# Kernel optimization log

Measured on AMD Instinct MI355X. Metric: run time of the kernel, lower is better.

The kernel has to match this reference:

```python
import jax, jax.numpy as jnp
import numpy as np

B, S, E, H, P = 8, 1024, 768, 12, 64
MASKED = True

def setup_inputs() -> dict:
    key = jax.random.key(0)
    k1, k2, k3, k4, k5 = jax.random.split(key, 5)
    scale = 0.02  # keep softmax logits in a sane range
    return {
        "x": jax.random.normal(k1, (B, 1, S, E), dtype=jnp.float32),
        "key_proj": jax.random.normal(k2, (H, E, P), dtype=jnp.float32) * scale,
        "value_proj": jax.random.normal(k3, (H, E, P), dtype=jnp.float32) * scale,
        "q_heads": jax.random.normal(k4, (H, S, S), dtype=jnp.float32) * scale,
        "lifting": jax.random.normal(k5, (1, H * P, E), dtype=jnp.float32) * scale,
    }

def reference(x, key_proj, value_proj, q_heads, lifting):
    # x: (B,1,S,E); key/value_proj: (H,E,P) -> broadcast matmul gives (B,H,S,P)
    k = jnp.matmul(x, key_proj)            # (B,H,S,P)
    v = jnp.matmul(x, value_proj)          # (B,H,S,P)
    # scores = (q_heads @ v) @ k^T, then transpose last two dims and scale
    qv = jnp.matmul(q_heads, v)            # (B,H,S,P)
    a_ts = jnp.matmul(qv, jnp.swapaxes(k, -2, -1))  # (B,H,S,S)
    a_ts = jnp.swapaxes(a_ts, -2, -1) / np.float32(np.sqrt(E))
    a_t = jax.nn.softmax(a_ts, axis=-1)
    if MASKED:
        a_t = jnp.tril(a_t)                 # causal lower-triangular mask
        a_t = a_t / jnp.sum(a_t, axis=-1, keepdims=True)  # renormalize rows
    attn = jnp.matmul(a_t, v)               # (B,H,S,P)
    attn = jnp.swapaxes(attn, 1, 2).reshape(B, S, H * P)  # (B,S,H*P)
    return jnp.matmul(attn, lifting)         # (B,S,E) via (1,H*P,E) broadcast
```

## Files before the change

kernel.cpp:

```cpp
#include <hip/hip_runtime.h>
#include <hip/hip_bf16.h>
#include <math.h>

#define B_ 8
#define S_ 1024
#define E_ 768
#define H_ 12
#define P_ 64

typedef __attribute__((ext_vector_type(8))) short bf16x8;
typedef __attribute__((ext_vector_type(4))) float f32x4;

__device__ __forceinline__ short f2bf(float f) {
    union { float f; unsigned u; } v; v.f = f;
    unsigned r = v.u + 0x7FFFu + ((v.u >> 16) & 1u);
    return (short)(r >> 16);
}

__device__ __forceinline__ short f2bf_hw(float f) {
    union { __hip_bfloat16 h; short s; } cv;
    cv.h = __float2bfloat16(f);
    return cv.s;
}

__device__ __forceinline__ void conv_T_body(
    const float* __restrict__ src0, short* __restrict__ dst0, int R, int C,
    int bx, int by, int bz, short (*T)[72])
{
    const int t = threadIdx.x;
    const int r0 = bx * 64, c0 = by * 64;
    const size_t bo = (size_t)bz * R * C;
    const float* src = src0 + bo;
    short* dst = dst0 + bo;
#pragma unroll
    for (int i = 0; i < 4; ++i) {
        int id = i * 256 + t;
        int r = id >> 4, c4 = id & 15;
        float4 f = *(const float4*)(src + (size_t)(r0 + r) * C + c0 + c4 * 4);
        T[c4 * 4 + 0][r] = f2bf(f.x);
        T[c4 * 4 + 1][r] = f2bf(f.y);
        T[c4 * 4 + 2][r] = f2bf(f.z);
        T[c4 * 4 + 3][r] = f2bf(f.w);
    }
    __syncthreads();
#pragma unroll
    for (int i = 0; i < 2; ++i) {
        int id = i * 256 + t;
        int cc = id >> 3, r8 = id & 7;
        *(uint4*)(dst + (size_t)(c0 + cc) * R + r0 + r8 * 8) = *(const uint4*)&T[cc][r8 * 8];
    }
}

__global__ __launch_bounds__(256) void conv_fused(
    const float* __restrict__ x, const float* __restrict__ qh,
    const float* __restrict__ kproj, const float* __restrict__ vproj,
    const float* __restrict__ lifting,
    short* __restrict__ xb, short* __restrict__ qhb,
    short* __restrict__ kTw, short* __restrict__ vTw, short* __restrict__ liftT)
{
    __shared__ short T[64][72];
    const int bid = (int)blockIdx.x;
    if (bid < 18432) {
        const float4* src; ushort4* dst; int idx;
        if (bid < 6144) { src = (const float4*)x;  dst = (ushort4*)xb;  idx = bid * 256 + threadIdx.x; }
        else            { src = (const float4*)qh; dst = (ushort4*)qhb; idx = (bid - 6144) * 256 + threadIdx.x; }
        float4 f = src[idx];
        ushort4 u;
        u.x = (unsigned short)f2bf(f.x);
        u.y = (unsigned short)f2bf(f.y);
        u.z = (unsigned short)f2bf(f.z);
        u.w = (unsigned short)f2bf(f.w);
        dst[idx] = u;
    } else if (bid < 18576) {
        int r = bid - 18432;
        conv_T_body(kproj, kTw, E_, P_, r % 12, 0, r / 12, T);
    } else if (bid < 18720) {
        int r = bid - 18576;
        conv_T_body(vproj, vTw, E_, P_, r % 12, 0, r / 12, T);
    } else {
        int r = bid - 18720;
        conv_T_body(lifting, liftT, E_, E_, r % 12, r / 12, 0, T);
    }
}

__device__ __forceinline__ void mfma_gemm_128x128(
    const short* __restrict__ A, int lda,
    const short* __restrict__ B0, const short* __restrict__ B1, int ldb, int K,
    short (*As)[72], short (*Bs)[72], f32x4 (&acc)[2][4])
{
    const int tid = threadIdx.x;
    const int w = tid >> 6, lane = tid & 63, quad = lane >> 4, ln = lane & 15;
    const int wm = w & 3, wn = w >> 2;

    const int r = tid >> 3, c8 = (tid & 7) * 8;
    const short* sA0 = A  + (size_t)r * lda + c8;
    const short* sA1 = A  + (size_t)(r + 64) * lda + c8;
    const short* sB0 = B0 + (size_t)r * ldb + c8;
    const short* sB1 = B1 + (size_t)r * ldb + c8;
    short* dA0 = &As[r][c8];
    short* dA1 = &As[r + 64][c8];
    short* dB0 = &Bs[r][c8];
    short* dB1 = &Bs[r + 64][c8];

    uint4 a0p = *(const uint4*)sA0;
    uint4 a1p = *(const uint4*)sA1;
    uint4 b0p = *(const uint4*)sB0;
    uint4 b1p = *(const uint4*)sB1;

    for (int k0 = 0; k0 < K; k0 += 64) {
        __syncthreads();
        *(uint4*)dA0 = a0p;
        *(uint4*)dA1 = a1p;
        *(uint4*)dB0 = b0p;
        *(uint4*)dB1 = b1p;
        if (k0 + 64 < K) {
            a0p = *(const uint4*)(sA0 + k0 + 64);
            a1p = *(const uint4*)(sA1 + k0 + 64);
            b0p = *(const uint4*)(sB0 + k0 + 64);
            b1p = *(const uint4*)(sB1 + k0 + 64);
        }
        __syncthreads();
#pragma unroll
        for (int kc = 0; kc < 2; ++kc) {
            bf16x8 a0 = *(const bf16x8*)&As[wm * 32 + ln][kc * 32 + quad * 8];
            bf16x8 a1 = *(const bf16x8*)&As[wm * 32 + 16 + ln][kc * 32 + quad * 8];
#pragma unroll
            for (int ni = 0; ni < 4; ++ni) {
                bf16x8 b = *(const bf16x8*)&Bs[wn * 64 + ni * 16 + ln][kc * 32 + quad * 8];
                acc[0][ni] = __builtin_amdgcn_mfma_f32_16x16x32_bf16(a0, b, acc[0][ni], 0, 0, 0);
                acc[1][ni] = __builtin_amdgcn_mfma_f32_16x16x32_bf16(a1, b, acc[1][ni], 0, 0, 0);
            }
        }
    }
}

__global__ __launch_bounds__(512, 2) void proj_kv_mfma(
    const short* __restrict__ xb,
    const short* __restrict__ kTw,
    const short* __restrict__ vTw,
    short* __restrict__ kb,
    short* __restrict__ vTb)
{
    __shared__ short As[128][72];
    __shared__ short Bs[128][72];
    const int tid = threadIdx.x;
    const int w = tid >> 6, lane = tid & 63, quad = lane >> 4, ln = lane & 15;
    const int wm = w & 3, wn = w >> 2;

    const int lid = (int)blockIdx.x;
    const int xcd = lid & 7, s = lid >> 3;
    const int mloc = s & 7, h = s >> 3;
    const int m0 = (xcd * 8 + mloc) * 128;

    f32x4 acc[2][4] = {};
    mfma_gemm_128x128(xb + (size_t)m0 * E_, E_,
                      kTw + (size_t)h * P_ * E_, vTw + (size_t)h * P_ * E_, E_, E_,
                      As, Bs, acc);

    const int b = m0 >> 10;
    const int sbase = (m0 & 1023) + wm * 32;
    if (wn == 0) {
        short* outp = kb + ((size_t)(b * H_ + h)) * S_ * P_;
#pragma unroll
        for (int mi = 0; mi < 2; ++mi)
#pragma unroll
            for (int ni = 0; ni < 4; ++ni)
#pragma unroll
                for (int r = 0; r < 4; ++r) {
                    int ss = sbase + mi * 16 + quad * 4 + r;
                    outp[(size_t)ss * P_ + ni * 16 + ln] = f2bf(acc[mi][ni][r]);
                }
    } else {
        short* outp = vTb + ((size_t)(b * H_ + h)) * P_ * S_;
#pragma unroll
        for (int mi = 0; mi < 2; ++mi)
#pragma unroll
            for (int ni = 0; ni < 4; ++ni) {
                int p = ni * 16 + ln;
                int ss = sbase + mi * 16 + quad * 4;
                ushort4 u;
                u.x = (unsigned short)f2bf(acc[mi][ni][0]);
                u.y = (unsigned short)f2bf(acc[mi][ni][1]);
                u.z = (unsigned short)f2bf(acc[mi][ni][2]);
                u.w = (unsigned short)f2bf(acc[mi][ni][3]);
                *(ushort4*)(outp + (size_t)p * S_ + ss) = u;
            }
    }
}

__global__ __launch_bounds__(512, 2) void qv_mfma(
    const short* __restrict__ qhb,
    const short* __restrict__ vTb,
    short* __restrict__ qvb)
{
    __shared__ short As[128][72];
    __shared__ short Bs[128][72];
    const int tid = threadIdx.x;
    const int w = tid >> 6, lane = tid & 63, quad = lane >> 4, ln = lane & 15;
    const int wm = w & 3, wn = w >> 2;

    const int lid = (int)blockIdx.x;
    const int xcd = lid & 7, s = lid >> 3;
    const int virt = xcd * 48 + s;
    const int h = virt >> 5;
    const int rem = virt & 31;
    const int mt = rem >> 2, bp = rem & 3;
    const int m0 = mt * 128;

    const short* Bv0 = vTb + (size_t)((bp * 2 + 0) * H_ + h) * P_ * S_;
    const short* Bv1 = vTb + (size_t)((bp * 2 + 1) * H_ + h) * P_ * S_;

    f32x4 acc[2][4] = {};
    mfma_gemm_128x128(qhb + (size_t)h * S_ * S_ + (size_t)m0 * S_, S_,
                      Bv0, Bv1, S_, S_, As, Bs, acc);

    const int b = bp * 2 + wn;
    short* outp = qvb + (size_t)(b * H_ + h) * S_ * P_;
#pragma unroll
    for (int mi = 0; mi < 2; ++mi)
#pragma unroll
        for (int ni = 0; ni < 4; ++ni)
#pragma unroll
            for (int r = 0; r < 4; ++r) {
                int ss = m0 + wm * 32 + mi * 16 + quad * 4 + r;
                outp[(size_t)ss * P_ + ni * 16 + ln] = f2bf(acc[mi][ni][r]);
            }
}

__global__ __launch_bounds__(512, 4) void flash_mfma(
    const short* __restrict__ kb,
    const short* __restrict__ qvb,
    const short* __restrict__ vTb,
    short* __restrict__ attn2)
{
    __shared__ short Ks[64][72];
    __shared__ short Vts[64][72];
    __shared__ short Ps[8][16][72];

    const int tid = threadIdx.x;
    const int w = tid >> 6, lane = tid & 63, quad = lane >> 4, ln = lane & 15;
    const int wq = w & 3;
    const int wsel = w >> 2;

    const int lid = (int)blockIdx.x;
    const int xcd = lid & 7, sl = lid >> 3;
    const int bh  = xcd * 12 + (sl >> 3);
    const int pair = sl & 7;
    const int qhi = 15 - pair;
    const int qb  = wsel ? pair : qhi;
    const int b = bh / H_, h = bh % H_;

    const short* Q  = kb  + (size_t)bh * S_ * P_ + ((size_t)qb * 64 + wq * 16) * P_;
    const short* K  = qvb + (size_t)bh * S_ * P_;
    const short* Vt = vTb + (size_t)bh * P_ * S_;

    bf16x8 qf[2];
    qf[0] = *(const bf16x8*)(Q + (size_t)ln * P_ + quad * 8);
    qf[1] = *(const bf16x8*)(Q + (size_t)ln * P_ + 32 + quad * 8);

    const int krow = tid >> 3, kc8 = (tid & 7) * 8;
    const short* Kst = K + (size_t)krow * P_ + kc8;
    const short* Vst = Vt + (size_t)krow * S_ + kc8;
    uint4 rK = *(const uint4*)Kst;
    uint4 rV = *(const uint4*)Vst;

    f32x4 o[4] = {};
    float l[4] = {};
    short (*Pw)[72] = Ps[w];
    const float c2 = 0.03608439182435161f * 1.4426950408889634f;
    const int rowbase = wq * 16;

    for (int jt = 0; jt <= qhi; ++jt) {
        __syncthreads();
        *(uint4*)&Ks[krow][kc8] = rK;
        *(uint4*)&Vts[krow][kc8] = rV;
        if (jt < qhi) {
            rK = *(const uint4*)(Kst + (size_t)(jt + 1) * 64 * P_);
            rV = *(const uint4*)(Vst + (jt + 1) * 64);
        }
        __syncthreads();

        if (jt <= qb) {
            const bool diag = (jt == qb);
            f32x4 s[4] = {};
#pragma unroll
            for (int kc = 0; kc < 2; ++kc)
#pragma unroll
                for (int ni = 0; ni < 4; ++ni) {
                    bf16x8 kf = *(const bf16x8*)&Ks[ni * 16 + ln][kc * 32 + quad * 8];
                    s[ni] = __builtin_amdgcn_mfma_f32_16x16x32_bf16(qf[kc], kf, s[ni], 0, 0, 0);
                }

#pragma unroll
            for (int r = 0; r < 4; ++r) {
                const int row = quad * 4 + r;
                float p[4];
#pragma unroll
                for (int ni = 0; ni < 4; ++ni) {
                    float v = __builtin_amdgcn_exp2f(c2 * s[ni][r]);
                    if (diag && (ni * 16 + ln) > (rowbase + row)) v = 0.f;
                    p[ni] = v;
                    l[r] += v;
                }
#pragma unroll
                for (int ni = 0; ni < 4; ++ni)
                    Pw[row][ni * 16 + ln] = f2bf_hw(p[ni]);
            }

#pragma unroll
            for (int kc = 0; kc < 2; ++kc) {
                bf16x8 pa = *(const bf16x8*)&Pw[ln][kc * 32 + quad * 8];
#pragma unroll
                for (int ni = 0; ni < 4; ++ni) {
                    bf16x8 vb = *(const bf16x8*)&Vts[ni * 16 + ln][kc * 32 + quad * 8];
                    o[ni] = __builtin_amdgcn_mfma_f32_16x16x32_bf16(pa, vb, o[ni], 0, 0, 0);
                }
            }
        }
    }

#pragma unroll
    for (int r = 0; r < 4; ++r) {
        float lv = l[r];
#pragma unroll
        for (int off = 1; off < 16; off <<= 1)
            lv += __shfl_xor(lv, off, 16);
        float inv = 1.0f / lv;
        int gi = qb * 64 + rowbase + quad * 4 + r;
#pragma unroll
        for (int ni = 0; ni < 4; ++ni)
            attn2[((size_t)b * S_ + gi) * (H_ * P_) + h * P_ + ni * 16 + ln] =
                f2bf(o[ni][r] * inv);
    }
}

__global__ __launch_bounds__(512, 2) void lift_mfma(
    const short* __restrict__ attn2,
    const short* __restrict__ liftT,
    float* __restrict__ outp)
{
    __shared__ short As[128][72];
    __shared__ short Bs[128][72];
    const int tid = threadIdx.x;
    const int w = tid >> 6, lane = tid & 63, quad = lane >> 4, ln = lane & 15;
    const int wm = w & 3, wn = w >> 2;

    const int lid = (int)blockIdx.x;
    const int xcd = lid & 7, s = lid >> 3;
    const int mloc = s & 7, np = s >> 3;
    const int m0 = (xcd * 8 + mloc) * 128;
    const int n0 = np * 128;

    f32x4 acc[2][4] = {};
    mfma_gemm_128x128(attn2 + (size_t)m0 * E_, E_,
                      liftT + (size_t)n0 * E_, liftT + (size_t)(n0 + 64) * E_, E_, E_,
                      As, Bs, acc);

#pragma unroll
    for (int mi = 0; mi < 2; ++mi)
#pragma unroll
        for (int ni = 0; ni < 4; ++ni)
#pragma unroll
            for (int r = 0; r < 4; ++r) {
                int m = m0 + wm * 32 + mi * 16 + quad * 4 + r;
                outp[(size_t)m * E_ + n0 + wn * 64 + ni * 16 + ln] = acc[mi][ni][r];
            }
}

extern "C" void kernel_launch(void* const* d_in, const int* in_sizes, int n_in,
                              void* d_out, int out_size, void* d_ws, size_t ws_size,
                              hipStream_t stream) {
    (void)in_sizes; (void)n_in; (void)out_size; (void)ws_size;
    const float* x       = (const float*)d_in[0];
    const float* kproj   = (const float*)d_in[1];
    const float* vproj   = (const float*)d_in[2];
    const float* qheads  = (const float*)d_in[3];
    const float* lifting = (const float*)d_in[4];
    float* out = (float*)d_out;

    short* ws = (short*)d_ws;
    const size_t N_X   = (size_t)B_ * S_ * E_;
    const size_t N_QH  = (size_t)H_ * S_ * S_;
    const size_t N_W   = (size_t)H_ * P_ * E_;
    const size_t N_L   = (size_t)E_ * E_;
    const size_t N_KV  = (size_t)B_ * H_ * S_ * P_;

    short* xb    = ws;                 ws += N_X;
    short* qhb   = ws;                 ws += N_QH;
    short* kTw   = ws;                 ws += N_W;
    short* vTw   = ws;                 ws += N_W;
    short* liftT = ws;                 ws += N_L;
    short* kb    = ws;                 ws += N_KV;
    short* vTb   = ws;                 ws += N_KV;
    short* qvb   = ws;                 ws += N_KV;
    short* attn2 = ws;                 ws += N_KV;

    conv_fused<<<dim3(18864), 256, 0, stream>>>(x, qheads, kproj, vproj, lifting,
                                                xb, qhb, kTw, vTw, liftT);
    proj_kv_mfma<<<dim3(768), 512, 0, stream>>>(xb, kTw, vTw, kb, vTb);
    qv_mfma<<<dim3(384), 512, 0, stream>>>(qhb, vTb, qvb);
    flash_mfma<<<dim3(768), 512, 0, stream>>>(kb, qvb, vTb, attn2);
    lift_mfma<<<dim3(384), 512, 0, stream>>>(attn2, liftT, out);
}
```

Measured before the change: 219.8 us.

## Rebalance flash kernel: split long query block's tail across both wave groups

Before, each block paired a short query tile (pair) with a long one (qhi), and the short tile's four waves sat idle once their causal range ended. Now both wave groups share the first phase. Once the short tile finishes, its waves write it out and switch to the long tile, with each group computing half of the key columns per KV tile. The two halves' partial O and l are then reduced through shared memory. This adds an extra barrier per tile in the second phase plus a final LDS reduction, and lowers launch bounds occupancy from 4 to 2.

```diff
diff --git a/kernel.cpp b/kernel.cpp
--- a/kernel.cpp
+++ b/kernel.cpp
@@ -227,7 +227,7 @@
             }
 }
 
-__global__ __launch_bounds__(512, 4) void flash_mfma(
+__global__ __launch_bounds__(512, 2) void flash_mfma(
     const short* __restrict__ kb,
     const short* __restrict__ qvb,
     const short* __restrict__ vTb,
@@ -235,7 +235,10 @@
 {
     __shared__ short Ks[64][72];
     __shared__ short Vts[64][72];
-    __shared__ short Ps[8][16][72];
+    __shared__ union PU {
+        short ps[8][16][72];
+        struct { float ored[4][16][68]; float lred[4][16][17]; } red;
+    } pu;
 
     const int tid = threadIdx.x;
     const int w = tid >> 6, lane = tid & 63, quad = lane >> 4, ln = lane & 15;
@@ -247,13 +250,14 @@
     const int bh  = xcd * 12 + (sl >> 3);
     const int pair = sl & 7;
     const int qhi = 15 - pair;
-    const int qb  = wsel ? pair : qhi;
     const int b = bh / H_, h = bh % H_;
 
-    const short* Q  = kb  + (size_t)bh * S_ * P_ + ((size_t)qb * 64 + wq * 16) * P_;
+    const short* Qbase = kb + (size_t)bh * S_ * P_;
     const short* K  = qvb + (size_t)bh * S_ * P_;
     const short* Vt = vTb + (size_t)bh * P_ * S_;
 
+    const int qb0 = wsel ? pair : qhi;
+    const short* Q = Qbase + ((size_t)qb0 * 64 + wq * 16) * P_;
     bf16x8 qf[2];
     qf[0] = *(const bf16x8*)(Q + (size_t)ln * P_ + quad * 8);
     qf[1] = *(const bf16x8*)(Q + (size_t)ln * P_ + 32 + quad * 8);
@@ -266,11 +270,78 @@
 
     f32x4 o[4] = {};
     float l[4] = {};
-    short (*Pw)[72] = Ps[w];
+    short (*Pw)[72] = pu.ps[w];
     const float c2 = 0.03608439182435161f * 1.4426950408889634f;
     const int rowbase = wq * 16;
 
-    for (int jt = 0; jt <= qhi; ++jt) {
+    for (int jt = 0; jt <= pair; ++jt) {
+        __syncthreads();
+        *(uint4*)&Ks[krow][kc8] = rK;
+        *(uint4*)&Vts[krow][kc8] = rV;
+        rK = *(const uint4*)(Kst + (size_t)(jt + 1) * 64 * P_);
+        rV = *(const uint4*)(Vst + (jt + 1) * 64);
+        __syncthreads();
+
+        const bool diag = (wsel == 1) && (jt == pair);
+        f32x4 s[4] = {};
+#pragma unroll
+        for (int kc = 0; kc < 2; ++kc)
+#pragma unroll
+            for (int ni = 0; ni < 4; ++ni) {
+                bf16x8 kf = *(const bf16x8*)&Ks[ni * 16 + ln][kc * 32 + quad * 8];
+                s[ni] = __builtin_amdgcn_mfma_f32_16x16x32_bf16(qf[kc], kf, s[ni], 0, 0, 0);
+            }
+#pragma unroll
+        for (int r = 0; r < 4; ++r) {
+            const int row = quad * 4 + r;
+            float p[4];
+#pragma unroll
+            for (int ni = 0; ni < 4; ++ni) {
+                float v = __builtin_amdgcn_exp2f(c2 * s[ni][r]);
+                if (diag && (ni * 16 + ln) > (rowbase + row)) v = 0.f;
+                p[ni] = v;
+                l[r] += v;
+            }
+#pragma unroll
+            for (int ni = 0; ni < 4; ++ni)
+                Pw[row][ni * 16 + ln] = f2bf_hw(p[ni]);
+        }
+#pragma unroll
+        for (int kc = 0; kc < 2; ++kc) {
+            bf16x8 pa = *(const bf16x8*)&Pw[ln][kc * 32 + quad * 8];
+#pragma unroll
+            for (int ni = 0; ni < 4; ++ni) {
+                bf16x8 vb = *(const bf16x8*)&Vts[ni * 16 + ln][kc * 32 + quad * 8];
+                o[ni] = __builtin_amdgcn_mfma_f32_16x16x32_bf16(pa, vb, o[ni], 0, 0, 0);
+            }
+        }
+    }
+
+    if (wsel == 1) {
+#pragma unroll
+        for (int r = 0; r < 4; ++r) {
+            float lv = l[r];
+#pragma unroll
+            for (int off = 1; off < 16; off <<= 1)
+                lv += __shfl_xor(lv, off, 16);
+            float inv = 1.0f / lv;
+            int gi = pair * 64 + rowbase + quad * 4 + r;
+#pragma unroll
+            for (int ni = 0; ni < 4; ++ni)
+                attn2[((size_t)b * S_ + gi) * (H_ * P_) + h * P_ + ni * 16 + ln] =
+                    f2bf(o[ni][r] * inv);
+        }
+#pragma unroll
+        for (int ni = 0; ni < 4; ++ni) o[ni] = (f32x4){0.f, 0.f, 0.f, 0.f};
+#pragma unroll
+        for (int r = 0; r < 4; ++r) l[r] = 0.f;
+        const short* Qh = Qbase + ((size_t)qhi * 64 + wq * 16) * P_;
+        qf[0] = *(const bf16x8*)(Qh + (size_t)ln * P_ + quad * 8);
+        qf[1] = *(const bf16x8*)(Qh + (size_t)ln * P_ + 32 + quad * 8);
+    }
+
+    short (*Pq)[72] = pu.ps[wq];
+    for (int jt = pair + 1; jt <= qhi; ++jt) {
         __syncthreads();
         *(uint4*)&Ks[krow][kc8] = rK;
         *(uint4*)&Vts[krow][kc8] = rV;
@@ -280,57 +351,75 @@
         }
         __syncthreads();
 
-        if (jt <= qb) {
-            const bool diag = (jt == qb);
-            f32x4 s[4] = {};
-#pragma unroll
-            for (int kc = 0; kc < 2; ++kc)
-#pragma unroll
-                for (int ni = 0; ni < 4; ++ni) {
-                    bf16x8 kf = *(const bf16x8*)&Ks[ni * 16 + ln][kc * 32 + quad * 8];
-                    s[ni] = __builtin_amdgcn_mfma_f32_16x16x32_bf16(qf[kc], kf, s[ni], 0, 0, 0);
-                }
-
-#pragma unroll
-            for (int r = 0; r < 4; ++r) {
-                const int row = quad * 4 + r;
-                float p[4];
-#pragma unroll
-                for (int ni = 0; ni < 4; ++ni) {
-                    float v = __builtin_amdgcn_exp2f(c2 * s[ni][r]);
-                    if (diag && (ni * 16 + ln) > (rowbase + row)) v = 0.f;
-                    p[ni] = v;
-                    l[r] += v;
-                }
-#pragma unroll
-                for (int ni = 0; ni < 4; ++ni)
-                    Pw[row][ni * 16 + ln] = f2bf_hw(p[ni]);
-            }
-
-#pragma unroll
-            for (int kc = 0; kc < 2; ++kc) {
-                bf16x8 pa = *(const bf16x8*)&Pw[ln][kc * 32 + quad * 8];
-#pragma unroll
-                for (int ni = 0; ni < 4; ++ni) {
-                    bf16x8 vb = *(const bf16x8*)&Vts[ni * 16 + ln][kc * 32 + quad * 8];
-                    o[ni] = __builtin_amdgcn_mfma_f32_16x16x32_bf16(pa, vb, o[ni], 0, 0, 0);
-                }
-            }
-        }
-    }
-
-#pragma unroll
-    for (int r = 0; r < 4; ++r) {
-        float lv = l[r];
-#pragma unroll
-        for (int off = 1; off < 16; off <<= 1)
-            lv += __shfl_xor(lv, off, 16);
-        float inv = 1.0f / lv;
-        int gi = qb * 64 + rowbase + quad * 4 + r;
-#pragma unroll
-        for (int ni = 0; ni < 4; ++ni)
-            attn2[((size_t)b * S_ + gi) * (H_ * P_) + h * P_ + ni * 16 + ln] =
-                f2bf(o[ni][r] * inv);
+        const bool diag = (jt == qhi);
+        f32x4 s2[2] = {};
+#pragma unroll
+        for (int kc = 0; kc < 2; ++kc)
+#pragma unroll
+            for (int nii = 0; nii < 2; ++nii) {
+                const int ni = wsel * 2 + nii;
+                bf16x8 kf = *(const bf16x8*)&Ks[ni * 16 + ln][kc * 32 + quad * 8];
+                s2[nii] = __builtin_amdgcn_mfma_f32_16x16x32_bf16(qf[kc], kf, s2[nii], 0, 0, 0);
+            }
+#pragma unroll
+        for (int r = 0; r < 4; ++r) {
+            const int row = quad * 4 + r;
+            float p[2];
+#pragma unroll
+            for (int nii = 0; nii < 2; ++nii) {
+                const int col = (wsel * 2 + nii) * 16 + ln;
+                float v = __builtin_amdgcn_exp2f(c2 * s2[nii][r]);
+                if (diag && col > (rowbase + row)) v = 0.f;
+                p[nii] = v;
+                l[r] += v;
+            }
+#pragma unroll
+            for (int nii = 0; nii < 2; ++nii)
+                Pq[row][(wsel * 2 + nii) * 16 + ln] = f2bf_hw(p[nii]);
+        }
+        __syncthreads();
+        {
+            bf16x8 pa = *(const bf16x8*)&Pq[ln][wsel * 32 + quad * 8];
+#pragma unroll
+            for (int ni = 0; ni < 4; ++ni) {
+                bf16x8 vb = *(const bf16x8*)&Vts[ni * 16 + ln][wsel * 32 + quad * 8];
+                o[ni] = __builtin_amdgcn_mfma_f32_16x16x32_bf16(pa, vb, o[ni], 0, 0, 0);
+            }
+        }
+    }
+
+    __syncthreads();
+    if (wsel == 1) {
+#pragma unroll
+        for (int r = 0; r < 4; ++r) {
+            pu.red.lred[wq][quad * 4 + r][ln] = l[r];
+#pragma unroll
+            for (int ni = 0; ni < 4; ++ni)
+                pu.red.ored[wq][quad * 4 + r][ni * 16 + ln] = o[ni][r];
+        }
+    }
+    __syncthreads();
+    if (wsel == 0) {
+#pragma unroll
+        for (int r = 0; r < 4; ++r) {
+            l[r] += pu.red.lred[wq][quad * 4 + r][ln];
+#pragma unroll
+            for (int ni = 0; ni < 4; ++ni)
+                o[ni][r] += pu.red.ored[wq][quad * 4 + r][ni * 16 + ln];
+        }
+#pragma unroll
+        for (int r = 0; r < 4; ++r) {
+            float lv = l[r];
+#pragma unroll
+            for (int off = 1; off < 16; off <<= 1)
+                lv += __shfl_xor(lv, off, 16);
+            float inv = 1.0f / lv;
+            int gi = qhi * 64 + rowbase + quad * 4 + r;
+#pragma unroll
+            for (int ni = 0; ni < 4; ++ni)
+                attn2[((size_t)b * S_ + gi) * (H_ * P_) + h * P_ + ni * 16 + ln] =
+                    f2bf(o[ni][r] * inv);
+        }
     }
 }
 
```

Measured after the change: 222.7 us. About the same (+1.3%).

## Fuse fp32-to-bf16 conversion of x and q_heads into GEMM tile loads

Applied to the files above, without the earlier changes.

Drops the separate conversion pass that wrote bf16 copies of x and q_heads to workspace. The projection and qv GEMMs now load fp32 A tiles directly and pack them to bf16 while staging into shared memory. This removes one full read and write of about 18M elements. The cost is that each GEMM reads twice the A bytes and does more conversion ALU work. The proj_kv block mapping is also reordered so heads vary fastest within an XCD, which changes how x tiles are reused in cache.

```diff
diff --git a/kernel.cpp b/kernel.cpp
--- a/kernel.cpp
+++ b/kernel.cpp
@@ -17,10 +17,22 @@
     return (short)(r >> 16);
 }
 
+__device__ __forceinline__ unsigned f2bf_u(float f) {
+    union { __hip_bfloat16 h; unsigned short s; } cv;
+    cv.h = __float2bfloat16(f);
+    return (unsigned)cv.s;
+}
 __device__ __forceinline__ short f2bf_hw(float f) {
-    union { __hip_bfloat16 h; short s; } cv;
-    cv.h = __float2bfloat16(f);
-    return cv.s;
+    return (short)f2bf_u(f);
+}
+
+__device__ __forceinline__ uint4 pack8(float4 a, float4 b) {
+    uint4 u;
+    u.x = f2bf_u(a.x) | (f2bf_u(a.y) << 16);
+    u.y = f2bf_u(a.z) | (f2bf_u(a.w) << 16);
+    u.z = f2bf_u(b.x) | (f2bf_u(b.y) << 16);
+    u.w = f2bf_u(b.z) | (f2bf_u(b.w) << 16);
+    return u;
 }
 
 __device__ __forceinline__ void conv_T_body(
@@ -52,39 +64,26 @@
 }
 
 __global__ __launch_bounds__(256) void conv_fused(
-    const float* __restrict__ x, const float* __restrict__ qh,
     const float* __restrict__ kproj, const float* __restrict__ vproj,
     const float* __restrict__ lifting,
-    short* __restrict__ xb, short* __restrict__ qhb,
     short* __restrict__ kTw, short* __restrict__ vTw, short* __restrict__ liftT)
 {
     __shared__ short T[64][72];
     const int bid = (int)blockIdx.x;
-    if (bid < 18432) {
-        const float4* src; ushort4* dst; int idx;
-        if (bid < 6144) { src = (const float4*)x;  dst = (ushort4*)xb;  idx = bid * 256 + threadIdx.x; }
-        else            { src = (const float4*)qh; dst = (ushort4*)qhb; idx = (bid - 6144) * 256 + threadIdx.x; }
-        float4 f = src[idx];
-        ushort4 u;
-        u.x = (unsigned short)f2bf(f.x);
-        u.y = (unsigned short)f2bf(f.y);
-        u.z = (unsigned short)f2bf(f.z);
-        u.w = (unsigned short)f2bf(f.w);
-        dst[idx] = u;
-    } else if (bid < 18576) {
-        int r = bid - 18432;
-        conv_T_body(kproj, kTw, E_, P_, r % 12, 0, r / 12, T);
-    } else if (bid < 18720) {
-        int r = bid - 18576;
+    if (bid < 144) {
+        conv_T_body(kproj, kTw, E_, P_, bid % 12, 0, bid / 12, T);
+    } else if (bid < 288) {
+        int r = bid - 144;
         conv_T_body(vproj, vTw, E_, P_, r % 12, 0, r / 12, T);
     } else {
-        int r = bid - 18720;
+        int r = bid - 288;
         conv_T_body(lifting, liftT, E_, E_, r % 12, r / 12, 0, T);
     }
 }
 
+template<bool AF32>
 __device__ __forceinline__ void mfma_gemm_128x128(
-    const short* __restrict__ A, int lda,
+    const void* __restrict__ Ap, int lda,
     const short* __restrict__ B0, const short* __restrict__ B1, int ldb, int K,
     short (*As)[72], short (*Bs)[72], f32x4 (&acc)[2][4])
 {
@@ -93,8 +92,10 @@
     const int wm = w & 3, wn = w >> 2;
 
     const int r = tid >> 3, c8 = (tid & 7) * 8;
-    const short* sA0 = A  + (size_t)r * lda + c8;
-    const short* sA1 = A  + (size_t)(r + 64) * lda + c8;
+    const float* fA0 = (const float*)Ap + (size_t)r * lda + c8;
+    const float* fA1 = (const float*)Ap + (size_t)(r + 64) * lda + c8;
+    const short* sA0 = (const short*)Ap + (size_t)r * lda + c8;
+    const short* sA1 = (const short*)Ap + (size_t)(r + 64) * lda + c8;
     const short* sB0 = B0 + (size_t)r * ldb + c8;
     const short* sB1 = B1 + (size_t)r * ldb + c8;
     short* dA0 = &As[r][c8];
@@ -102,20 +103,40 @@
     short* dB0 = &Bs[r][c8];
     short* dB1 = &Bs[r + 64][c8];
 
-    uint4 a0p = *(const uint4*)sA0;
-    uint4 a1p = *(const uint4*)sA1;
-    uint4 b0p = *(const uint4*)sB0;
-    uint4 b1p = *(const uint4*)sB1;
+    float4 a0lo, a0hi, a1lo, a1hi;
+    uint4 a0p, a1p;
+    uint4 b0p, b1p;
+    if (AF32) {
+        a0lo = *(const float4*)fA0; a0hi = *(const float4*)(fA0 + 4);
+        a1lo = *(const float4*)fA1; a1hi = *(const float4*)(fA1 + 4);
+    } else {
+        a0p = *(const uint4*)sA0;
+        a1p = *(const uint4*)sA1;
+    }
+    b0p = *(const uint4*)sB0;
+    b1p = *(const uint4*)sB1;
 
     for (int k0 = 0; k0 < K; k0 += 64) {
         __syncthreads();
-        *(uint4*)dA0 = a0p;
-        *(uint4*)dA1 = a1p;
+        if (AF32) {
+            *(uint4*)dA0 = pack8(a0lo, a0hi);
+            *(uint4*)dA1 = pack8(a1lo, a1hi);
+        } else {
+            *(uint4*)dA0 = a0p;
+            *(uint4*)dA1 = a1p;
+        }
         *(uint4*)dB0 = b0p;
         *(uint4*)dB1 = b1p;
         if (k0 + 64 < K) {
-            a0p = *(const uint4*)(sA0 + k0 + 64);
-            a1p = *(const uint4*)(sA1 + k0 + 64);
+            if (AF32) {
+                a0lo = *(const float4*)(fA0 + k0 + 64);
+                a0hi = *(const float4*)(fA0 + k0 + 68);
+                a1lo = *(const float4*)(fA1 + k0 + 64);
+                a1hi = *(const float4*)(fA1 + k0 + 68);
+            } else {
+                a0p = *(const uint4*)(sA0 + k0 + 64);
+                a1p = *(const uint4*)(sA1 + k0 + 64);
+            }
             b0p = *(const uint4*)(sB0 + k0 + 64);
             b1p = *(const uint4*)(sB1 + k0 + 64);
         }
@@ -135,7 +156,7 @@
 }
 
 __global__ __launch_bounds__(512, 2) void proj_kv_mfma(
-    const short* __restrict__ xb,
+    const float* __restrict__ x,
     const short* __restrict__ kTw,
     const short* __restrict__ vTw,
     short* __restrict__ kb,
@@ -149,13 +170,13 @@
 
     const int lid = (int)blockIdx.x;
     const int xcd = lid & 7, s = lid >> 3;
-    const int mloc = s & 7, h = s >> 3;
+    const int h = s % 12, mloc = s / 12;
     const int m0 = (xcd * 8 + mloc) * 128;
 
     f32x4 acc[2][4] = {};
-    mfma_gemm_128x128(xb + (size_t)m0 * E_, E_,
-                      kTw + (size_t)h * P_ * E_, vTw + (size_t)h * P_ * E_, E_, E_,
-                      As, Bs, acc);
+    mfma_gemm_128x128<true>(x + (size_t)m0 * E_, E_,
+                            kTw + (size_t)h * P_ * E_, vTw + (size_t)h * P_ * E_, E_, E_,
+                            As, Bs, acc);
 
     const int b = m0 >> 10;
     const int sbase = (m0 & 1023) + wm * 32;
@@ -189,7 +210,7 @@
 }
 
 __global__ __launch_bounds__(512, 2) void qv_mfma(
-    const short* __restrict__ qhb,
+    const float* __restrict__ qheads,
     const short* __restrict__ vTb,
     short* __restrict__ qvb)
 {
@@ -211,8 +232,8 @@
     const short* Bv1 = vTb + (size_t)((bp * 2 + 1) * H_ + h) * P_ * S_;
 
     f32x4 acc[2][4] = {};
-    mfma_gemm_128x128(qhb + (size_t)h * S_ * S_ + (size_t)m0 * S_, S_,
-                      Bv0, Bv1, S_, S_, As, Bs, acc);
+    mfma_gemm_128x128<true>(qheads + (size_t)h * S_ * S_ + (size_t)m0 * S_, S_,
+                            Bv0, Bv1, S_, S_, As, Bs, acc);
 
     const int b = bp * 2 + wn;
     short* outp = qvb + (size_t)(b * H_ + h) * S_ * P_;
@@ -352,9 +373,9 @@
     const int n0 = np * 128;
 
     f32x4 acc[2][4] = {};
-    mfma_gemm_128x128(attn2 + (size_t)m0 * E_, E_,
-                      liftT + (size_t)n0 * E_, liftT + (size_t)(n0 + 64) * E_, E_, E_,
-                      As, Bs, acc);
+    mfma_gemm_128x128<false>(attn2 + (size_t)m0 * E_, E_,
+                             liftT + (size_t)n0 * E_, liftT + (size_t)(n0 + 64) * E_, E_, E_,
+                             As, Bs, acc);
 
 #pragma unroll
     for (int mi = 0; mi < 2; ++mi)
@@ -379,14 +400,10 @@
     float* out = (float*)d_out;
 
     short* ws = (short*)d_ws;
-    const size_t N_X   = (size_t)B_ * S_ * E_;
-    const size_t N_QH  = (size_t)H_ * S_ * S_;
     const size_t N_W   = (size_t)H_ * P_ * E_;
     const size_t N_L   = (size_t)E_ * E_;
     const size_t N_KV  = (size_t)B_ * H_ * S_ * P_;
 
-    short* xb    = ws;                 ws += N_X;
-    short* qhb   = ws;                 ws += N_QH;
     short* kTw   = ws;                 ws += N_W;
     short* vTw   = ws;                 ws += N_W;
     short* liftT = ws;                 ws += N_L;
@@ -395,10 +412,9 @@
     short* qvb   = ws;                 ws += N_KV;
     short* attn2 = ws;                 ws += N_KV;
 
-    conv_fused<<<dim3(18864), 256, 0, stream>>>(x, qheads, kproj, vproj, lifting,
-                                                xb, qhb, kTw, vTw, liftT);
-    proj_kv_mfma<<<dim3(768), 512, 0, stream>>>(xb, kTw, vTw, kb, vTb);
-    qv_mfma<<<dim3(384), 512, 0, stream>>>(qhb, vTb, qvb);
+    conv_fused<<<dim3(432), 256, 0, stream>>>(kproj, vproj, lifting, kTw, vTw, liftT);
+    proj_kv_mfma<<<dim3(768), 512, 0, stream>>>(x, kTw, vTw, kb, vTb);
+    qv_mfma<<<dim3(384), 512, 0, stream>>>(qheads, vTb, qvb);
     flash_mfma<<<dim3(768), 512, 0, stream>>>(kb, qvb, vTb, attn2);
     lift_mfma<<<dim3(384), 512, 0, stream>>>(attn2, liftT, out);
 }
```

Result: slower. 233.7 us (+6.3%).
